# Kernel optimization log

Hardware: AMD Instinct MI355X
Metric: run time of the kernel (lower is better)

## Reference

```python
import jax, jax.numpy as jnp
import numpy as np

B, T, S, A = 4, 10, 6, 6
HID, L, IMG = 512, 6, 128
NCH = 16  # spatial-softmax channels
_px, _py = np.meshgrid(np.linspace(-1.0, 1.0, IMG), np.linspace(-1.0, 1.0, IMG))
POSX = jnp.asarray(_px.reshape(-1), jnp.float32)
POSY = jnp.asarray(_py.reshape(-1), jnp.float32)


def _conv_relu(x, w, b):
    y = jax.lax.conv_general_dilated(x, w, (1, 1), 'SAME',
                                     dimension_numbers=('NCHW', 'OIHW', 'NCHW'))
    return jax.nn.relu(y + b[None, :, None, None])


def _cnn_ss(x, ws, bs):
    for w, b in zip(ws, bs):
        x = _conv_relu(x, w, b)
    n = x.shape[0]
    attn = jax.nn.softmax(x.reshape(n, NCH, -1), axis=-1)  # (n, 16, H*W)
    ex = attn @ POSX  # (n, 16)
    ey = attn @ POSY
    return jnp.stack([ex, ey], axis=-1).reshape(n, 2 * NCH)  # (n, 32)


def _lstm_cell(x, h, c, wih, whh, bih, bhh):
    g = x @ wih.T + bih + h @ whh.T + bhh
    i, f, gg, o = jnp.split(g, 4, axis=-1)  # torch LSTMCell gate order i,f,g,o
    c2 = jax.nn.sigmoid(f) * c + jax.nn.sigmoid(i) * jnp.tanh(gg)
    h2 = jax.nn.sigmoid(o) * jnp.tanh(c2)
    return h2, c2


def setup_inputs() -> dict:
    key = jax.random.key(0)
    ks = iter(jax.random.split(key, 64))

    def nrm(shape, s=0.05):
        return jax.random.normal(next(ks), shape, dtype=jnp.float32) * s

    inp = {
        'seq_img_main': nrm((B, T, 3, IMG, IMG), 1.0),
        'seq_img_secondary': nrm((B, T, 3, IMG, IMG), 1.0),
        'seq_states': nrm((B, T, S), 1.0),
    }
    chans = [(32, 3), (64, 32), (128, 64), (16, 128)]
    for cam in ('m', 's'):
        for j, (o, ci) in enumerate(chans):
            inp[f'{cam}_w{j}'] = nrm((o, ci, 3, 3))
            inp[f'{cam}_b{j}'] = nrm((o,))
    in0, inr = S + 64, HID + 64  # 70 and 576
    inp['wih0'] = nrm((4 * HID, in0)); inp['whh0'] = nrm((4 * HID, HID))
    inp['bih0'] = nrm((4 * HID,)); inp['bhh0'] = nrm((4 * HID,))
    inp['wih_r'] = nrm((L - 1, 4 * HID, inr)); inp['whh_r'] = nrm((L - 1, 4 * HID, HID))
    inp['bih_r'] = nrm((L - 1, 4 * HID)); inp['bhh_r'] = nrm((L - 1, 4 * HID))
    inp['out_w'] = nrm((A, inr)); inp['out_b'] = nrm((A,))
    return inp


def reference(seq_img_main, seq_img_secondary, seq_states,
              m_w0, m_b0, m_w1, m_b1, m_w2, m_b2, m_w3, m_b3,
              s_w0, s_b0, s_w1, s_b1, s_w2, s_b2, s_w3, s_b3,
              wih0, whh0, bih0, bhh0, wih_r, whh_r, bih_r, bhh_r,
              out_w, out_b):
    b, t = seq_img_main.shape[:2]
    fm = _cnn_ss(seq_img_main.reshape(b * t, 3, IMG, IMG),
                 [m_w0, m_w1, m_w2, m_w3], [m_b0, m_b1, m_b2, m_b3])
    fs = _cnn_ss(seq_img_secondary.reshape(b * t, 3, IMG, IMG),
                 [s_w0, s_w1, s_w2, s_w3], [s_b0, s_b1, s_b2, s_b3])
    img = jnp.concatenate([fm, fs], axis=-1).reshape(b, t, 64)  # (B,T,64)

    h0 = jnp.zeros((L, b, HID), jnp.float32)
    c0 = jnp.zeros((L, b, HID), jnp.float32)

    def step(carry, xt):
        h, c = carry
        st, im = xt  # (B,S), (B,64)
        x = jnp.concatenate([st, im], axis=-1)
        hn, cn = _lstm_cell(x, h[0], c[0], wih0, whh0, bih0, bhh0)
        hs, cs = [hn], [cn]
        for l in range(L - 1):
            x = jnp.concatenate([hs[-1], im], axis=-1)
            hl, cl = _lstm_cell(x, h[l + 1], c[l + 1],
                                wih_r[l], whh_r[l], bih_r[l], bhh_r[l])
            hs.append(hl); cs.append(cl)
        out = jnp.concatenate([hs[-1], im], axis=-1) @ out_w.T + out_b
        return (jnp.stack(hs), jnp.stack(cs)), out

    _, outs = jax.lax.scan(step, (h0, c0),
                           (seq_states.transpose(1, 0, 2), img.transpose(1, 0, 2)))
    return outs.transpose(1, 0, 2)  # (B,T,A)
```

## Files before the change

kernel.cpp:

```cpp
#include <hip/hip_runtime.h>
#include <hip/hip_bf16.h>
#include <math.h>

typedef __hip_bfloat16 bf16;
typedef short bf16x8 __attribute__((ext_vector_type(8)));
typedef float f32x4 __attribute__((ext_vector_type(4)));

static constexpr int HWPX = 16384;

__device__ inline float sigmoidf_(float x) { return 1.0f / (1.0f + expf(-x)); }
__device__ inline float bflo(unsigned u) { return __uint_as_float(u << 16); }
__device__ inline float bfhi(unsigned u) { return __uint_as_float(u & 0xffff0000u); }
__device__ inline int swz(int x) { return (x ^ (x >> 2)) & 3; }

__device__ inline void gll16(const bf16* g, short* l) {
    __builtin_amdgcn_global_load_lds(
        (const __attribute__((address_space(1))) void*)g,
        (__attribute__((address_space(3))) void*)l, 16, 0, 0);
}

__global__ __launch_bounds__(256) void prep_lstm_k(
    const float* __restrict__ wih0, const float* __restrict__ whh0,
    const float* __restrict__ wihr, const float* __restrict__ whhr,
    bf16* __restrict__ d0, bf16* __restrict__ d1,
    bf16* __restrict__ d2, bf16* __restrict__ d3)
{
    const size_t nA = 2048ull * 72, nB = 2048ull * 512;
    const size_t nC = 5ull * 2048 * 576, nD = 5ull * 2048 * 512;
    for (size_t i = blockIdx.x * 256ull + threadIdx.x; i < nA + nB + nC + nD;
         i += (size_t)gridDim.x * 256) {
        if (i < nA) {
            int c = (int)(i % 72), r = (int)(i / 72);
            d0[i] = __float2bfloat16(c < 70 ? wih0[(size_t)r * 70 + c] : 0.f);
        } else if (i < nA + nB) {
            size_t k = i - nA; d1[k] = __float2bfloat16(whh0[k]);
        } else if (i < nA + nB + nC) {
            size_t k = i - nA - nB; d2[k] = __float2bfloat16(wihr[k]);
        } else {
            size_t k = i - nA - nB - nC; d3[k] = __float2bfloat16(whhr[k]);
        }
    }
}

struct ConvW {
    const float* src[8];
    bf16* dst[8];
};

__global__ __launch_bounds__(256) void prep_conv_k(ConvW a)
{
    const int sizes[4] = {3072, 18432, 73728, 18432};
    const int cins[4] = {3, 32, 64, 128};
    const int couts[4] = {32, 64, 128, 16};
    int total = 2 * 113664;
    for (int idx = blockIdx.x * 256 + threadIdx.x; idx < total; idx += gridDim.x * 256) {
        int i = idx, cam = 0;
        if (i >= 113664) { cam = 1; i -= 113664; }
        int layer = 0;
        while (layer < 3 && i >= sizes[layer]) { i -= sizes[layer]; ++layer; }
        const float* w = a.src[cam * 4 + layer];
        bf16* d = a.dst[cam * 4 + layer];
        if (layer == 0) {
            int k = i & 31, co = (i >> 5) & 31, ky = i >> 10;
            int kx = k >> 3, c = k & 7;
            float v = (kx < 3 && c < 3) ? w[((co * 3 + c) * 3 + ky) * 3 + kx] : 0.f;
            d[i] = __float2bfloat16(v);
        } else {
            int CIN = cins[layer], COUT = couts[layer], KC = CIN / 32;
            int e = i & 7;
            int t2 = i >> 3;
            int co = t2 % COUT;
            int t3 = t2 / COUT;
            int q = t3 & 3;
            int t4 = t3 >> 2;
            int kc = t4 % KC;
            int tap = t4 / KC;
            d[i] = __float2bfloat16(w[((size_t)(co * CIN + kc * 32 + q * 8 + e)) * 9 + tap]);
        }
    }
}

__global__ __launch_bounds__(256) void conv0_nhwc(
    const float* __restrict__ srcm, const float* __restrict__ srcs,
    const bf16* __restrict__ w0m, const bf16* __restrict__ w0s,
    const float* __restrict__ bm, const float* __restrict__ bs,
    bf16* __restrict__ out, int c0)
{
    const int y = blockIdx.x;
    const int cam = blockIdx.y;
    const int img = blockIdx.z;
    const int ci_ = cam * gridDim.z + img;
    const float* inImg = (cam ? srcs : srcm) + (size_t)(c0 + img) * 3 * HWPX;
    const bf16* wT0 = cam ? w0s : w0m;
    const float* bias = cam ? bs : bm;
    const int tid = threadIdx.x;
    const int wave = tid >> 6, lane = tid & 63;
    const int wm = wave & 1, wn = wave >> 1;
    const int q = lane >> 4, n16 = lane & 15;

    __shared__ short smem[3 * 130 * 16];

    for (int d = tid; d < 3 * 130; d += 256) {
        int x = d % 130, r = d / 130;
        int yy = y + r - 1, xx = x - 1;
        bf16 v8[8];
#pragma unroll
        for (int c = 0; c < 8; ++c) v8[c] = __float2bfloat16(0.f);
        if ((unsigned)yy < 128u && (unsigned)xx < 128u) {
            int o = yy * 128 + xx;
            v8[0] = __float2bfloat16(inImg[o]);
            v8[1] = __float2bfloat16(inImg[HWPX + o]);
            v8[2] = __float2bfloat16(inImg[2 * HWPX + o]);
        }
        *(bf16x8*)(void*)&smem[(r * 130 + x) * 16] = *(bf16x8*)(void*)v8;
        *(bf16x8*)(void*)&smem[(r * 130 + x) * 16 + 8] = (bf16x8)0;
    }
    __syncthreads();

    f32x4 acc[4];
#pragma unroll
    for (int nt = 0; nt < 4; ++nt) acc[nt] = f32x4{0.f, 0.f, 0.f, 0.f};

    const int co = wm * 16 + n16;
#pragma unroll
    for (int ky = 0; ky < 3; ++ky) {
        bf16x8 aF = *(const bf16x8*)(const void*)(wT0 + ((size_t)(ky * 32 + co) * 32) + q * 8);
#pragma unroll
        for (int nt = 0; nt < 4; ++nt) {
            int x = (wn * 4 + nt) * 16 + n16;
            int off = (q < 3) ? (ky * 130 + x + q) * 16 : (ky * 130 + x) * 16 + 8;
            bf16x8 bF = *(const bf16x8*)(const void*)&smem[off];
            acc[nt] = __builtin_amdgcn_mfma_f32_16x16x32_bf16(aF, bF, acc[nt], 0, 0, 0);
        }
    }

    int co0 = wm * 16 + q * 4;
#pragma unroll
    for (int nt = 0; nt < 4; ++nt) {
        int x = (wn * 4 + nt) * 16 + n16;
        bf16 tmp[4];
#pragma unroll
        for (int r = 0; r < 4; ++r) {
            float v = acc[nt][r] + bias[co0 + r];
            tmp[r] = __float2bfloat16(v > 0.f ? v : 0.f);
        }
        *reinterpret_cast<uint2*>(out + ((size_t)ci_ * HWPX + y * 128 + x) * 32 + co0)
            = *reinterpret_cast<uint2*>(tmp);
    }
}

template <int CIN, int COUT>
__global__ __launch_bounds__(256, 4) void conv2r(
    const bf16* __restrict__ in, const bf16* __restrict__ wTm,
    const bf16* __restrict__ wTs, const float* __restrict__ bm,
    const float* __restrict__ bs, bf16* __restrict__ out,
    const char* __restrict__ zpage)
{
    constexpr int KC = CIN / 32;
    constexpr int NB = (KC > 1) ? 2 : 1;
    constexpr int MW = COUT / 32;
    constexpr int SLOTS = 4 * 264;

    const int y0 = (blockIdx.x >> 1) * 2;
    const int x0 = (blockIdx.x & 1) * 64;
    const int cam = blockIdx.y;
    const int img = blockIdx.z;
    const int ci_ = cam * gridDim.z + img;
    const bf16* wT = cam ? wTs : wTm;
    const float* bias = cam ? bs : bm;
    const int tid = threadIdx.x;
    const int wave = tid >> 6, lane = tid & 63;
    const int wrow = wave >> 1, wm = wave & 1;
    const int q = lane >> 4, n16 = lane & 15;

    __shared__ short smem[NB][SLOTS * 8];
    const bf16* inImg = in + (size_t)ci_ * HWPX * CIN;

    const bf16* sptr[5];
#pragma unroll
    for (int it = 0; it < 5; ++it) {
        int s = it * 256 + tid;
        int r = s / 264, s2 = s - r * 264;
        int sx = s2 >> 2;
        int g = (s2 & 3) ^ swz(sx);
        int yy = y0 + r - 1, xx = x0 + sx - 1;
        bool ok = (s < SLOTS) && ((unsigned)yy < 128u) && ((unsigned)xx < 128u);
        sptr[it] = ok ? inImg + ((size_t)yy * 128 + xx) * CIN + g * 8
                      : (const bf16*)(zpage + (tid & 255) * 16);
    }
    auto stage = [&](int kc, int buf) {
#pragma unroll
        for (int it = 0; it < 5; ++it) {
            if (it * 256 + tid < SLOTS)
                gll16(sptr[it] + kc * 32, &smem[buf][it * 2048 + wave * 512]);
        }
    };

    f32x4 acc[MW][4];
#pragma unroll
    for (int mt = 0; mt < MW; ++mt)
#pragma unroll
        for (int nt = 0; nt < 4; ++nt) acc[mt][nt] = f32x4{0.f, 0.f, 0.f, 0.f};

    stage(0, 0);
    for (int kc = 0; kc < KC; ++kc) {
        __syncthreads();
        if (kc + 1 < KC) stage(kc + 1, (kc + 1) % NB);
        const short* sb = smem[kc % NB];
#pragma unroll
        for (int ky = 0; ky < 3; ++ky) {
#pragma unroll
            for (int kx = 0; kx < 3; ++kx) {
                bf16x8 aF[MW];
#pragma unroll
                for (int mt = 0; mt < MW; ++mt) {
                    int co = (wm * MW + mt) * 16 + n16;
                    aF[mt] = *(const bf16x8*)(const void*)(wT +
                        ((((size_t)(ky * 3 + kx) * KC + kc) * 4 + q) * COUT + co) * 8);
                }
#pragma unroll
                for (int nt = 0; nt < 4; ++nt) {
                    int xt = nt * 16 + n16 + kx;
                    int slot = (wrow + ky) * 264 + xt * 4 + (q ^ swz(xt));
                    bf16x8 bF = *(const bf16x8*)(const void*)&sb[slot * 8];
#pragma unroll
                    for (int mt = 0; mt < MW; ++mt)
                        acc[mt][nt] = __builtin_amdgcn_mfma_f32_16x16x32_bf16(
                            aF[mt], bF, acc[mt][nt], 0, 0, 0);
                }
            }
        }
    }

    const int y = y0 + wrow;
#pragma unroll
    for (int mt = 0; mt < MW; ++mt) {
        int co0 = (wm * MW + mt) * 16 + q * 4;
#pragma unroll
        for (int nt = 0; nt < 4; ++nt) {
            int x = x0 + nt * 16 + n16;
            bf16 tmp[4];
#pragma unroll
            for (int r = 0; r < 4; ++r) {
                float v = acc[mt][nt][r] + bias[co0 + r];
                tmp[r] = __float2bfloat16(v > 0.f ? v : 0.f);
            }
            *reinterpret_cast<uint2*>(out + ((size_t)ci_ * HWPX + y * 128 + x) * COUT + co0)
                = *reinterpret_cast<uint2*>(tmp);
        }
    }
}

__global__ __launch_bounds__(256, 6) void conv4_xs(
    const bf16* __restrict__ in, const bf16* __restrict__ wTm,
    const bf16* __restrict__ wTs, const float* __restrict__ bm,
    const float* __restrict__ bs,
    float* __restrict__ partial,
    const char* __restrict__ zpage, int c0)
{
    constexpr int CIN = 128, COUT = 16, KC = 4;
    constexpr int SLOTS = 3 * 66 * 4;
    const int y = blockIdx.x >> 1;
    const int xh = blockIdx.x & 1;
    const int x0 = xh * 64;
    const int cam = blockIdx.y;
    const int img = blockIdx.z;
    const int ci_ = cam * gridDim.z + img;
    const int gimg = cam * 40 + c0 + img;
    const bf16* wT = cam ? wTs : wTm;
    const float* bias = cam ? bs : bm;
    const int tid = threadIdx.x;
    const int wave = tid >> 6, lane = tid & 63;
    const int q = lane >> 4, n16 = lane & 15;

    __shared__ short smem[2][SLOTS * 8];
    __shared__ float sred[3][4][16];
    const bf16* inImg = in + (size_t)ci_ * HWPX * CIN;

    const bf16* sptr[4];
#pragma unroll
    for (int it = 0; it < 4; ++it) {
        int s = it * 256 + tid;
        int r = s / 264, s2 = s - r * 264;
        int sx = s2 >> 2;
        int g = (s2 & 3) ^ swz(sx);
        int yy = y + r - 1, xx = x0 + sx - 1;
        bool ok = (s < SLOTS) && ((unsigned)yy < 128u) && ((unsigned)xx < 128u);
        sptr[it] = ok ? inImg + ((size_t)yy * 128 + xx) * CIN + g * 8
                      : (const bf16*)(zpage + (tid & 255) * 16);
    }
    auto stage = [&](int kc, int buf) {
#pragma unroll
        for (int it = 0; it < 4; ++it) {
            if (it * 256 + tid < SLOTS)
                gll16(sptr[it] + kc * 32, &smem[buf][it * 2048 + wave * 512]);
        }
    };

    f32x4 acc = f32x4{0.f, 0.f, 0.f, 0.f};

    stage(0, 0);
    for (int kc = 0; kc < KC; ++kc) {
        __syncthreads();
        if (kc + 1 < KC) stage(kc + 1, (kc + 1) & 1);
        const short* sb = smem[kc & 1];
#pragma unroll
        for (int ky = 0; ky < 3; ++ky) {
#pragma unroll
            for (int kx = 0; kx < 3; ++kx) {
                bf16x8 aF = *(const bf16x8*)(const void*)(wT +
                    ((((size_t)(ky * 3 + kx) * KC + kc) * 4 + q) * COUT + n16) * 8);
                int xt = wave * 16 + n16 + kx;
                int slot = xt * 4 + (q ^ swz(xt));
                bf16x8 bF = *(const bf16x8*)(const void*)&sb[ky * 2112 + slot * 8];
                acc = __builtin_amdgcn_mfma_f32_16x16x32_bf16(aF, bF, acc, 0, 0, 0);
            }
        }
    }

    float v[4];
    int x = x0 + wave * 16 + n16;
    float px = -1.f + (2.f / 127.f) * x;
#pragma unroll
    for (int r = 0; r < 4; ++r) {
        float t = acc[r] + bias[q * 4 + r];
        v[r] = t > 0.f ? t : 0.f;
    }
    float M[4];
#pragma unroll
    for (int r = 0; r < 4; ++r) {
        M[r] = v[r];
        M[r] = fmaxf(M[r], __shfl_xor(M[r], 1));
        M[r] = fmaxf(M[r], __shfl_xor(M[r], 2));
        M[r] = fmaxf(M[r], __shfl_xor(M[r], 4));
        M[r] = fmaxf(M[r], __shfl_xor(M[r], 8));
    }
    if (n16 == 0)
#pragma unroll
        for (int r = 0; r < 4; ++r) sred[0][wave][q * 4 + r] = M[r];
    __syncthreads();
#pragma unroll
    for (int r = 0; r < 4; ++r) {
        M[r] = fmaxf(fmaxf(sred[0][0][q * 4 + r], sred[0][1][q * 4 + r]),
                     fmaxf(sred[0][2][q * 4 + r], sred[0][3][q * 4 + r]));
    }
    float s[4], sx[4];
#pragma unroll
    for (int r = 0; r < 4; ++r) {
        float e = expf(v[r] - M[r]);
        s[r] = e; sx[r] = e * px;
        s[r] += __shfl_xor(s[r], 1);  sx[r] += __shfl_xor(sx[r], 1);
        s[r] += __shfl_xor(s[r], 2);  sx[r] += __shfl_xor(sx[r], 2);
        s[r] += __shfl_xor(s[r], 4);  sx[r] += __shfl_xor(sx[r], 4);
        s[r] += __shfl_xor(s[r], 8);  sx[r] += __shfl_xor(sx[r], 8);
    }
    __syncthreads();
    if (n16 == 0)
#pragma unroll
        for (int r = 0; r < 4; ++r) {
            sred[1][wave][q * 4 + r] = s[r];
            sred[2][wave][q * 4 + r] = sx[r];
        }
    __syncthreads();
    if (tid < 16) {
        float S = sred[1][0][tid] + sred[1][1][tid] + sred[1][2][tid] + sred[1][3][tid];
        float SX = sred[2][0][tid] + sred[2][1][tid] + sred[2][2][tid] + sred[2][3][tid];
        float Mv = fmaxf(fmaxf(sred[0][0][tid], sred[0][1][tid]),
                         fmaxf(sred[0][2][tid], sred[0][3][tid]));
        float* pp = partial + (((size_t)gimg * 16 + tid) * 256 + (y * 2 + xh)) * 4;
        pp[0] = Mv; pp[1] = S; pp[2] = SX;
    }
}

__global__ __launch_bounds__(256) void ssmerge_k(
    const float* __restrict__ partial, float* __restrict__ featm,
    float* __restrict__ feats)
{
    const int img = blockIdx.x;
    const int cam = img / 40, li = img % 40;
    float* feat = cam ? feats : featm;
    const int tid = threadIdx.x;
    const int co = tid >> 4, s = tid & 15;
    const float* base = partial + ((size_t)img * 16 + co) * 256 * 4;
    float M = -1e30f, S = 0.f, SX = 0.f, SY = 0.f;
    for (int i = s; i < 256; i += 16) {
        float m = base[i * 4], sv = base[i * 4 + 1], sxv = base[i * 4 + 2];
        float py = -1.f + (2.f / 127.f) * (i >> 1);
        float Mn = fmaxf(M, m);
        float w0 = expf(M - Mn), w1 = expf(m - Mn);
        S = S * w0 + sv * w1;
        SX = SX * w0 + sxv * w1;
        SY = SY * w0 + sv * py * w1;
        M = Mn;
    }
#pragma unroll
    for (int mask = 1; mask < 16; mask <<= 1) {
        float Mo = __shfl_xor(M, mask), So = __shfl_xor(S, mask);
        float SXo = __shfl_xor(SX, mask), SYo = __shfl_xor(SY, mask);
        float Mn = fmaxf(M, Mo);
        float w0 = expf(M - Mn), w1 = expf(Mo - Mn);
        S = S * w0 + So * w1; SX = SX * w0 + SXo * w1; SY = SY * w0 + SYo * w1;
        M = Mn;
    }
    if (s == 0) {
        feat[(size_t)li * 32 + 2 * co] = SX / S;
        feat[(size_t)li * 32 + 2 * co + 1] = SY / S;
    }
}

__device__ inline float imgfeat(const float* featm, const float* feats,
                                int b, int t, int k)
{
    int idx = (b * 10 + t) * 32;
    return k < 32 ? featm[idx + k] : feats[idx + k - 32];
}

__global__ __launch_bounds__(256) void lstm_diag_k(
    const bf16* __restrict__ wih0p, const bf16* __restrict__ whh0b,
    const bf16* __restrict__ wihrb, const bf16* __restrict__ whhrb,
    const float* __restrict__ bih0, const float* __restrict__ bhh0,
    const float* __restrict__ bihr, const float* __restrict__ bhhr,
    const float* __restrict__ states,
    const float* __restrict__ featm, const float* __restrict__ feats,
    float* __restrict__ hAll, float* __restrict__ cAll,
    const float* __restrict__ out_w, const float* __restrict__ out_b,
    float* __restrict__ out, int d)
{
    const int l = blockIdx.y;
    const int tid = threadIdx.x;

    if (l == 6) {
        int t = d - 6;
        if (t < 0 || t >= 10 || blockIdx.x != 0) return;
        const float* h5 = hAll + ((size_t)(t + 1) * 6 + 5) * 2048;
        int p = tid >> 3, sub = tid & 7;
        if (p >= 24) return;
        int b = p / 6, a = p % 6;
        const float* wr = out_w + a * 576;
        float acc = 0.f;
        for (int k = sub; k < 512; k += 8) acc += wr[k] * h5[b * 512 + k];
        for (int k = sub; k < 64; k += 8) acc += wr[512 + k] * imgfeat(featm, feats, b, t, k);
        acc += __shfl_xor(acc, 1);
        acc += __shfl_xor(acc, 2);
        acc += __shfl_xor(acc, 4);
        if (sub == 0) out[(b * 10 + t) * 6 + a] = acc + out_b[a];
        return;
    }

    const int t = d - l;
    if (t < 0 || t >= 10) return;

    const bf16 *wih, *whh;
    const float *bih, *bhh;
    int K1;
    if (l == 0) { wih = wih0p; whh = whh0b; bih = bih0; bhh = bhh0; K1 = 72; }
    else {
        wih = wihrb + (size_t)(l - 1) * 2048 * 576;
        whh = whhrb + (size_t)(l - 1) * 2048 * 512;
        bih = bihr + (l - 1) * 2048;
        bhh = bhhr + (l - 1) * 2048;
        K1 = 576;
    }
    const float* hprev = (l == 0) ? nullptr : hAll + ((size_t)(t + 1) * 6 + (l - 1)) * 2048;
    const float* hold  = hAll + ((size_t)t * 6 + l) * 2048;
    float* hnew        = hAll + ((size_t)(t + 1) * 6 + l) * 2048;
    float* cst         = cAll + (size_t)l * 2048;

    const int XS = K1 + 512;
    __shared__ float xs[4 * 1088];
    for (int i = tid; i < 4 * XS; i += 256) {
        int b = i / XS, k = i - b * XS;
        float v;
        if (k < K1) {
            if (hprev) v = (k < 512) ? hprev[b * 512 + k]
                                     : imgfeat(featm, feats, b, t, k - 512);
            else       v = (k < 6) ? states[(b * 10 + t) * 6 + k]
                                   : (k < 70 ? imgfeat(featm, feats, b, t, k - 6) : 0.f);
        } else {
            v = hold[b * 512 + (k - K1)];
        }
        xs[b * XS + k] = v;
    }
    __syncthreads();

    const int b = tid >> 6;
    const int jloc = (tid >> 4) & 3;
    const int sub = tid & 15;
    const int j = blockIdx.x * 4 + jloc;
    const float* xb = xs + b * XS;
    const float* hp = xb + K1;
    float dg[4] = {0.f, 0.f, 0.f, 0.f};
    const int nb1 = K1 >> 3;
#pragma unroll
    for (int r = 0; r < 4; ++r) {
        const uint4* w1 = reinterpret_cast<const uint4*>(wih + (size_t)(j + r * 512) * K1);
        for (int g = sub; g < nb1; g += 16) {
            uint4 u = w1[g]; const float* xp = xb + g * 8;
            dg[r] += bflo(u.x) * xp[0] + bfhi(u.x) * xp[1] + bflo(u.y) * xp[2] + bfhi(u.y) * xp[3]
                   + bflo(u.z) * xp[4] + bfhi(u.z) * xp[5] + bflo(u.w) * xp[6] + bfhi(u.w) * xp[7];
        }
        const uint4* w2 = reinterpret_cast<const uint4*>(whh + (size_t)(j + r * 512) * 512);
        for (int g = sub; g < 64; g += 16) {
            uint4 u = w2[g]; const float* xp = hp + g * 8;
            dg[r] += bflo(u.x) * xp[0] + bfhi(u.x) * xp[1] + bflo(u.y) * xp[2] + bfhi(u.y) * xp[3]
                   + bflo(u.z) * xp[4] + bfhi(u.z) * xp[5] + bflo(u.w) * xp[6] + bfhi(u.w) * xp[7];
        }
    }
#pragma unroll
    for (int r = 0; r < 4; ++r) {
        dg[r] += __shfl_xor(dg[r], 1);
        dg[r] += __shfl_xor(dg[r], 2);
        dg[r] += __shfl_xor(dg[r], 4);
        dg[r] += __shfl_xor(dg[r], 8);
    }
    if (sub == 0) {
        float gi = dg[0] + bih[j] + bhh[j];
        float gf = dg[1] + bih[j + 512] + bhh[j + 512];
        float gg = dg[2] + bih[j + 1024] + bhh[j + 1024];
        float go = dg[3] + bih[j + 1536] + bhh[j + 1536];
        float cp = cst[b * 512 + j];
        float c2 = sigmoidf_(gf) * cp + sigmoidf_(gi) * tanhf(gg);
        float h2 = sigmoidf_(go) * tanhf(c2);
        cst[b * 512 + j] = c2;
        hnew[b * 512 + j] = h2;
    }
}

extern "C" void kernel_launch(void* const* d_in, const int* in_sizes, int n_in,
                              void* d_out, int out_size, void* d_ws, size_t ws_size,
                              hipStream_t stream)
{
    const float* seq_m = (const float*)d_in[0];
    const float* seq_s = (const float*)d_in[1];
    const float* states = (const float*)d_in[2];
    const float *cw[2][4], *cb[2][4];
    for (int cam = 0; cam < 2; ++cam)
        for (int j = 0; j < 4; ++j) {
            cw[cam][j] = (const float*)d_in[3 + cam * 8 + j * 2];
            cb[cam][j] = (const float*)d_in[3 + cam * 8 + j * 2 + 1];
        }
    const float* wih0  = (const float*)d_in[19];
    const float* whh0  = (const float*)d_in[20];
    const float* bih0  = (const float*)d_in[21];
    const float* bhh0  = (const float*)d_in[22];
    const float* wih_r = (const float*)d_in[23];
    const float* whh_r = (const float*)d_in[24];
    const float* bih_r = (const float*)d_in[25];
    const float* bhh_r = (const float*)d_in[26];
    const float* out_w = (const float*)d_in[27];
    const float* out_b = (const float*)d_in[28];
    float* out = (float*)d_out;

    char* wsc = (char*)d_ws;
    auto carve = [&](size_t bytes) {
        char* p = wsc;
        wsc += (bytes + 255) & ~(size_t)255;
        return p;
    };
    float* featm = (float*)carve(40 * 32 * 4);
    float* feats = (float*)carve(40 * 32 * 4);
    float* hAll  = (float*)carve((size_t)11 * 6 * 2048 * 4);
    float* cAll  = (float*)carve((size_t)6 * 2048 * 4);
    char*  zpage = carve(8192);
    float* partial = (float*)carve((size_t)80 * 16 * 256 * 4 * 4);
    const int wtElts[4] = {3072, 18432, 73728, 18432};
    bf16* wT[2][4];
    for (int cam = 0; cam < 2; ++cam)
        for (int j = 0; j < 4; ++j) wT[cam][j] = (bf16*)carve(wtElts[j] * 2);
    bf16* wih0p = (bf16*)carve((size_t)2048 * 72 * 2);
    bf16* whh0b = (bf16*)carve((size_t)2048 * 512 * 2);
    bf16* wihrb = (bf16*)carve((size_t)5 * 2048 * 576 * 2);
    bf16* whhrb = (bf16*)carve((size_t)5 * 2048 * 512 * 2);

    size_t used = (size_t)(wsc - (char*)d_ws);
    size_t rem = ws_size > used ? ws_size - used : 0;
    int CHI = 1;
    const int cands[7] = {20, 10, 8, 5, 4, 2, 1};
    for (int i = 0; i < 7; ++i) {
        size_t need = (size_t)2 * cands[i] * (128 + 64) * HWPX * 2;
        if (need <= rem) { CHI = cands[i]; break; }
    }
    bf16* bufA = (bf16*)carve((size_t)2 * CHI * HWPX * 128 * 2);
    bf16* bufB = (bf16*)carve((size_t)2 * CHI * HWPX * 64 * 2);

    hipMemsetAsync(hAll, 0, 6 * 2048 * 4, stream);
    hipMemsetAsync(cAll, 0, 6 * 2048 * 4, stream);
    hipMemsetAsync(zpage, 0, 8192, stream);

    prep_lstm_k<<<2048, 256, 0, stream>>>(wih0, whh0, wih_r, whh_r,
                                          wih0p, whh0b, wihrb, whhrb);
    ConvW cwArg;
    for (int cam = 0; cam < 2; ++cam)
        for (int j = 0; j < 4; ++j) {
            cwArg.src[cam * 4 + j] = cw[cam][j];
            cwArg.dst[cam * 4 + j] = wT[cam][j];
        }
    prep_conv_k<<<888, 256, 0, stream>>>(cwArg);

    for (int c0 = 0; c0 < 40; c0 += CHI) {
        int ch = (40 - c0) < CHI ? (40 - c0) : CHI;
        conv0_nhwc<<<dim3(128, 2, ch), 256, 0, stream>>>(
            seq_m, seq_s, wT[0][0], wT[1][0], cb[0][0], cb[1][0], bufA, c0);
        conv2r<32, 64><<<dim3(128, 2, ch), 256, 0, stream>>>(
            bufA, wT[0][1], wT[1][1], cb[0][1], cb[1][1], bufB, zpage);
        conv2r<64, 128><<<dim3(128, 2, ch), 256, 0, stream>>>(
            bufB, wT[0][2], wT[1][2], cb[0][2], cb[1][2], bufA, zpage);
        conv4_xs<<<dim3(256, 2, ch), 256, 0, stream>>>(
            bufA, wT[0][3], wT[1][3], cb[0][3], cb[1][3], partial, zpage, c0);
    }
    ssmerge_k<<<80, 256, 0, stream>>>(partial, featm, feats);

    for (int d = 0; d < 16; ++d) {
        lstm_diag_k<<<dim3(128, 7), 256, 0, stream>>>(
            wih0p, whh0b, wihrb, whhrb, bih0, bhh0, bih_r, bhh_r,
            states, featm, feats, hAll, cAll, out_w, out_b, out, d);
    }
}
```

Measured before the change: 1.139 ms.

## Fuse LSTM diagonal launches into one cooperative kernel with grid sync

```diff
diff --git a/kernel.cpp b/kernel.cpp
--- a/kernel.cpp
+++ b/kernel.cpp
@@ -1,6 +1,9 @@
 #include <hip/hip_runtime.h>
 #include <hip/hip_bf16.h>
+#include <hip/hip_cooperative_groups.h>
 #include <math.h>
+
+namespace cg = cooperative_groups;
 
 typedef __hip_bfloat16 bf16;
 typedef short bf16x8 __attribute__((ext_vector_type(8)));
@@ -526,6 +529,130 @@
     }
 }
 
+__global__ __launch_bounds__(256) void lstm_coop_k(
+    const bf16* __restrict__ wih0p, const bf16* __restrict__ whh0b,
+    const bf16* __restrict__ wihrb, const bf16* __restrict__ whhrb,
+    const float* __restrict__ bih0, const float* __restrict__ bhh0,
+    const float* __restrict__ bihr, const float* __restrict__ bhhr,
+    const float* __restrict__ states,
+    const float* __restrict__ featm, const float* __restrict__ feats,
+    float* __restrict__ hAll, float* __restrict__ cAll,
+    const float* __restrict__ out_w, const float* __restrict__ out_b,
+    float* __restrict__ out)
+{
+    cg::grid_group grid = cg::this_grid();
+    const int l = blockIdx.x >> 7;
+    const int bx = blockIdx.x & 127;
+    const int tid = threadIdx.x;
+
+    const bf16 *wih = nullptr, *whh = nullptr;
+    const float *bih = nullptr, *bhh = nullptr;
+    int K1 = 0;
+    if (l == 0) { wih = wih0p; whh = whh0b; bih = bih0; bhh = bhh0; K1 = 72; }
+    else if (l < 6) {
+        wih = wihrb + (size_t)(l - 1) * 2048 * 576;
+        whh = whhrb + (size_t)(l - 1) * 2048 * 512;
+        bih = bihr + (l - 1) * 2048;
+        bhh = bhhr + (l - 1) * 2048;
+        K1 = 576;
+    }
+    const int XS = K1 + 512;
+    float* cst = cAll + (size_t)l * 2048;
+
+    __shared__ float xs[4 * 1088];
+
+    for (int d = 0; d < 16; ++d) {
+        if (l == 6) {
+            int t = d - 6;
+            if (t >= 0 && t < 10 && bx == 0) {
+                const float* h5 = hAll + ((size_t)(t + 1) * 6 + 5) * 2048;
+                int p = tid >> 3, sub = tid & 7;
+                if (p < 24) {
+                    int b = p / 6, a = p % 6;
+                    const float* wr = out_w + a * 576;
+                    float acc = 0.f;
+                    for (int k = sub; k < 512; k += 8) acc += wr[k] * h5[b * 512 + k];
+                    for (int k = sub; k < 64; k += 8)
+                        acc += wr[512 + k] * imgfeat(featm, feats, b, t, k);
+                    acc += __shfl_xor(acc, 1);
+                    acc += __shfl_xor(acc, 2);
+                    acc += __shfl_xor(acc, 4);
+                    if (sub == 0) out[(b * 10 + t) * 6 + a] = acc + out_b[a];
+                }
+            }
+        } else {
+            const int t = d - l;
+            if (t >= 0 && t < 10) {
+                const float* hprev = (l == 0) ? nullptr
+                                   : hAll + ((size_t)(t + 1) * 6 + (l - 1)) * 2048;
+                const float* hold  = hAll + ((size_t)t * 6 + l) * 2048;
+                float* hnew        = hAll + ((size_t)(t + 1) * 6 + l) * 2048;
+
+                for (int i = tid; i < 4 * XS; i += 256) {
+                    int b = i / XS, k = i - b * XS;
+                    float v;
+                    if (k < K1) {
+                        if (hprev) v = (k < 512) ? hprev[b * 512 + k]
+                                                 : imgfeat(featm, feats, b, t, k - 512);
+                        else       v = (k < 6) ? states[(b * 10 + t) * 6 + k]
+                                               : (k < 70 ? imgfeat(featm, feats, b, t, k - 6) : 0.f);
+                    } else {
+                        v = hold[b * 512 + (k - K1)];
+                    }
+                    xs[b * XS + k] = v;
+                }
+                __syncthreads();
+
+                const int b = tid >> 6;
+                const int jloc = (tid >> 4) & 3;
+                const int sub = tid & 15;
+                const int j = bx * 4 + jloc;
+                const float* xb = xs + b * XS;
+                const float* hp = xb + K1;
+                float dg[4] = {0.f, 0.f, 0.f, 0.f};
+                const int nb1 = K1 >> 3;
+#pragma unroll
+                for (int r = 0; r < 4; ++r) {
+                    const uint4* w1 = reinterpret_cast<const uint4*>(wih + (size_t)(j + r * 512) * K1);
+                    for (int g = sub; g < nb1; g += 16) {
+                        uint4 u = w1[g]; const float* xp = xb + g * 8;
+                        dg[r] += bflo(u.x) * xp[0] + bfhi(u.x) * xp[1] + bflo(u.y) * xp[2] + bfhi(u.y) * xp[3]
+                               + bflo(u.z) * xp[4] + bfhi(u.z) * xp[5] + bflo(u.w) * xp[6] + bfhi(u.w) * xp[7];
+                    }
+                    const uint4* w2 = reinterpret_cast<const uint4*>(whh + (size_t)(j + r * 512) * 512);
+                    for (int g = sub; g < 64; g += 16) {
+                        uint4 u = w2[g]; const float* xp = hp + g * 8;
+                        dg[r] += bflo(u.x) * xp[0] + bfhi(u.x) * xp[1] + bflo(u.y) * xp[2] + bfhi(u.y) * xp[3]
+                               + bflo(u.z) * xp[4] + bfhi(u.z) * xp[5] + bflo(u.w) * xp[6] + bfhi(u.w) * xp[7];
+                    }
+                }
+#pragma unroll
+                for (int r = 0; r < 4; ++r) {
+                    dg[r] += __shfl_xor(dg[r], 1);
+                    dg[r] += __shfl_xor(dg[r], 2);
+                    dg[r] += __shfl_xor(dg[r], 4);
+                    dg[r] += __shfl_xor(dg[r], 8);
+                }
+                if (sub == 0) {
+                    float gi = dg[0] + bih[j] + bhh[j];
+                    float gf = dg[1] + bih[j + 512] + bhh[j + 512];
+                    float gg = dg[2] + bih[j + 1024] + bhh[j + 1024];
+                    float go = dg[3] + bih[j + 1536] + bhh[j + 1536];
+                    float cp = cst[b * 512 + j];
+                    float c2 = sigmoidf_(gf) * cp + sigmoidf_(gi) * tanhf(gg);
+                    float h2 = sigmoidf_(go) * tanhf(c2);
+                    cst[b * 512 + j] = c2;
+                    hnew[b * 512 + j] = h2;
+                }
+            }
+        }
+        if (d < 15) {
+            __threadfence();
+            grid.sync();
+        }
+    }
+}
+
 extern "C" void kernel_launch(void* const* d_in, const int* in_sizes, int n_in,
                               void* d_out, int out_size, void* d_ws, size_t ws_size,
                               hipStream_t stream)
@@ -575,8 +702,8 @@
     size_t used = (size_t)(wsc - (char*)d_ws);
     size_t rem = ws_size > used ? ws_size - used : 0;
     int CHI = 1;
-    const int cands[7] = {20, 10, 8, 5, 4, 2, 1};
-    for (int i = 0; i < 7; ++i) {
+    const int cands[6] = {10, 8, 5, 4, 2, 1};
+    for (int i = 0; i < 6; ++i) {
         size_t need = (size_t)2 * cands[i] * (128 + 64) * HWPX * 2;
         if (need <= rem) { CHI = cands[i]; break; }
     }
@@ -610,9 +737,21 @@
     }
     ssmerge_k<<<80, 256, 0, stream>>>(partial, featm, feats);
 
-    for (int d = 0; d < 16; ++d) {
-        lstm_diag_k<<<dim3(128, 7), 256, 0, stream>>>(
-            wih0p, whh0b, wihrb, whhrb, bih0, bhh0, bih_r, bhh_r,
-            states, featm, feats, hAll, cAll, out_w, out_b, out, d);
-    }
-}
+    void* kargs[] = {
+        (void*)&wih0p, (void*)&whh0b, (void*)&wihrb, (void*)&whhrb,
+        (void*)&bih0, (void*)&bhh0, (void*)&bih_r, (void*)&bhh_r,
+        (void*)&states, (void*)&featm, (void*)&feats,
+        (void*)&hAll, (void*)&cAll,
+        (void*)&out_w, (void*)&out_b, (void*)&out
+    };
+    hipError_t ce = hipLaunchCooperativeKernel(
+        reinterpret_cast<void*>(lstm_coop_k), dim3(896), dim3(256),
+        kargs, 0, stream);
+    if (ce != hipSuccess) {
+        for (int d = 0; d < 16; ++d) {
+            lstm_diag_k<<<dim3(128, 7), 256, 0, stream>>>(
+                wih0p, whh0b, wihrb, whhrb, bih0, bhh0, bih_r, bhh_r,
+                states, featm, feats, hAll, cAll, out_w, out_b, out, d);
+        }
+    }
+}
```

Result: slower. 3.875 ms (+240.2%).

## Replace per-diagonal LSTM launches with persistent flag-synchronized pipeline kernel

Applied to the files above, without the earlier changes.

```diff
diff --git a/kernel.cpp b/kernel.cpp
--- a/kernel.cpp
+++ b/kernel.cpp
@@ -7,6 +7,7 @@
 typedef float f32x4 __attribute__((ext_vector_type(4)));
 
 static constexpr int HWPX = 16384;
+static constexpr int NBL  = 64;
 
 __device__ inline float sigmoidf_(float x) { return 1.0f / (1.0f + expf(-x)); }
 __device__ inline float bflo(unsigned u) { return __uint_as_float(u << 16); }
@@ -17,6 +18,19 @@
     __builtin_amdgcn_global_load_lds(
         (const __attribute__((address_space(1))) void*)g,
         (__attribute__((address_space(3))) void*)l, 16, 0, 0);
+}
+
+__device__ inline void flag_wait(int* p, int target) {
+    if (threadIdx.x == 0) {
+        while (__hip_atomic_load(p, __ATOMIC_ACQUIRE, __HIP_MEMORY_SCOPE_AGENT) < target)
+            __builtin_amdgcn_s_sleep(2);
+    }
+    __syncthreads();
+}
+__device__ inline void flag_post(int* p) {
+    __syncthreads();
+    if (threadIdx.x == 0)
+        __hip_atomic_fetch_add(p, 1, __ATOMIC_RELEASE, __HIP_MEMORY_SCOPE_AGENT);
 }
 
 __global__ __launch_bounds__(256) void prep_lstm_k(
@@ -415,7 +429,7 @@
     return k < 32 ? featm[idx + k] : feats[idx + k - 32];
 }
 
-__global__ __launch_bounds__(256) void lstm_diag_k(
+__global__ __launch_bounds__(256) void lstm_pipe_k(
     const bf16* __restrict__ wih0p, const bf16* __restrict__ whh0b,
     const bf16* __restrict__ wihrb, const bf16* __restrict__ whhrb,
     const float* __restrict__ bih0, const float* __restrict__ bhh0,
@@ -424,31 +438,34 @@
     const float* __restrict__ featm, const float* __restrict__ feats,
     float* __restrict__ hAll, float* __restrict__ cAll,
     const float* __restrict__ out_w, const float* __restrict__ out_b,
-    float* __restrict__ out, int d)
-{
-    const int l = blockIdx.y;
+    float* __restrict__ out, int* __restrict__ cnt)
+{
+    const int gb = blockIdx.x;
     const int tid = threadIdx.x;
 
-    if (l == 6) {
-        int t = d - 6;
-        if (t < 0 || t >= 10 || blockIdx.x != 0) return;
-        const float* h5 = hAll + ((size_t)(t + 1) * 6 + 5) * 2048;
-        int p = tid >> 3, sub = tid & 7;
-        if (p >= 24) return;
-        int b = p / 6, a = p % 6;
-        const float* wr = out_w + a * 576;
-        float acc = 0.f;
-        for (int k = sub; k < 512; k += 8) acc += wr[k] * h5[b * 512 + k];
-        for (int k = sub; k < 64; k += 8) acc += wr[512 + k] * imgfeat(featm, feats, b, t, k);
-        acc += __shfl_xor(acc, 1);
-        acc += __shfl_xor(acc, 2);
-        acc += __shfl_xor(acc, 4);
-        if (sub == 0) out[(b * 10 + t) * 6 + a] = acc + out_b[a];
+    if (gb == 6 * NBL) {
+        for (int t = 0; t < 10; ++t) {
+            flag_wait(&cnt[(5 * 10 + t) * 32], NBL);
+            const float* h5 = hAll + ((size_t)(t + 1) * 6 + 5) * 2048;
+            int p = tid >> 3, sub = tid & 7;
+            if (p < 24) {
+                int b = p / 6, a = p % 6;
+                const float* wr = out_w + a * 576;
+                float acc = 0.f;
+                for (int k = sub; k < 512; k += 8) acc += wr[k] * h5[b * 512 + k];
+                for (int k = sub; k < 64; k += 8)
+                    acc += wr[512 + k] * imgfeat(featm, feats, b, t, k);
+                acc += __shfl_xor(acc, 1);
+                acc += __shfl_xor(acc, 2);
+                acc += __shfl_xor(acc, 4);
+                if (sub == 0) out[(b * 10 + t) * 6 + a] = acc + out_b[a];
+            }
+        }
         return;
     }
 
-    const int t = d - l;
-    if (t < 0 || t >= 10) return;
+    const int l = gb / NBL;
+    const int bx = gb % NBL;
 
     const bf16 *wih, *whh;
     const float *bih, *bhh;
@@ -461,68 +478,78 @@
         bhh = bhhr + (l - 1) * 2048;
         K1 = 576;
     }
-    const float* hprev = (l == 0) ? nullptr : hAll + ((size_t)(t + 1) * 6 + (l - 1)) * 2048;
-    const float* hold  = hAll + ((size_t)t * 6 + l) * 2048;
-    float* hnew        = hAll + ((size_t)(t + 1) * 6 + l) * 2048;
-    float* cst         = cAll + (size_t)l * 2048;
-
     const int XS = K1 + 512;
+    float* cst = cAll + (size_t)l * 2048;
+
+    const int b = tid >> 6;
+    const int lane = tid & 63;
+    const int jloc = lane >> 3;
+    const int sub = lane & 7;
+    const int j = bx * 8 + jloc;
+    const int nb1 = K1 >> 3;
+
     __shared__ float xs[4 * 1088];
-    for (int i = tid; i < 4 * XS; i += 256) {
-        int b = i / XS, k = i - b * XS;
-        float v;
-        if (k < K1) {
-            if (hprev) v = (k < 512) ? hprev[b * 512 + k]
-                                     : imgfeat(featm, feats, b, t, k - 512);
-            else       v = (k < 6) ? states[(b * 10 + t) * 6 + k]
-                                   : (k < 70 ? imgfeat(featm, feats, b, t, k - 6) : 0.f);
-        } else {
-            v = hold[b * 512 + (k - K1)];
-        }
-        xs[b * XS + k] = v;
-    }
-    __syncthreads();
-
-    const int b = tid >> 6;
-    const int jloc = (tid >> 4) & 3;
-    const int sub = tid & 15;
-    const int j = blockIdx.x * 4 + jloc;
-    const float* xb = xs + b * XS;
-    const float* hp = xb + K1;
-    float dg[4] = {0.f, 0.f, 0.f, 0.f};
-    const int nb1 = K1 >> 3;
-#pragma unroll
-    for (int r = 0; r < 4; ++r) {
-        const uint4* w1 = reinterpret_cast<const uint4*>(wih + (size_t)(j + r * 512) * K1);
-        for (int g = sub; g < nb1; g += 16) {
-            uint4 u = w1[g]; const float* xp = xb + g * 8;
-            dg[r] += bflo(u.x) * xp[0] + bfhi(u.x) * xp[1] + bflo(u.y) * xp[2] + bfhi(u.y) * xp[3]
-                   + bflo(u.z) * xp[4] + bfhi(u.z) * xp[5] + bflo(u.w) * xp[6] + bfhi(u.w) * xp[7];
-        }
-        const uint4* w2 = reinterpret_cast<const uint4*>(whh + (size_t)(j + r * 512) * 512);
-        for (int g = sub; g < 64; g += 16) {
-            uint4 u = w2[g]; const float* xp = hp + g * 8;
-            dg[r] += bflo(u.x) * xp[0] + bfhi(u.x) * xp[1] + bflo(u.y) * xp[2] + bfhi(u.y) * xp[3]
-                   + bflo(u.z) * xp[4] + bfhi(u.z) * xp[5] + bflo(u.w) * xp[6] + bfhi(u.w) * xp[7];
-        }
-    }
-#pragma unroll
-    for (int r = 0; r < 4; ++r) {
-        dg[r] += __shfl_xor(dg[r], 1);
-        dg[r] += __shfl_xor(dg[r], 2);
-        dg[r] += __shfl_xor(dg[r], 4);
-        dg[r] += __shfl_xor(dg[r], 8);
-    }
-    if (sub == 0) {
-        float gi = dg[0] + bih[j] + bhh[j];
-        float gf = dg[1] + bih[j + 512] + bhh[j + 512];
-        float gg = dg[2] + bih[j + 1024] + bhh[j + 1024];
-        float go = dg[3] + bih[j + 1536] + bhh[j + 1536];
-        float cp = cst[b * 512 + j];
-        float c2 = sigmoidf_(gf) * cp + sigmoidf_(gi) * tanhf(gg);
-        float h2 = sigmoidf_(go) * tanhf(c2);
-        cst[b * 512 + j] = c2;
-        hnew[b * 512 + j] = h2;
+
+    for (int t = 0; t < 10; ++t) {
+        if (t > 0) flag_wait(&cnt[(l * 10 + t - 1) * 32], NBL);
+        if (l > 0) flag_wait(&cnt[((l - 1) * 10 + t) * 32], NBL);
+
+        const float* hprev = (l == 0) ? nullptr
+                           : hAll + ((size_t)(t + 1) * 6 + (l - 1)) * 2048;
+        const float* hold  = hAll + ((size_t)t * 6 + l) * 2048;
+        float* hnew        = hAll + ((size_t)(t + 1) * 6 + l) * 2048;
+
+        for (int i = tid; i < 4 * XS; i += 256) {
+            int bb = i / XS, k = i - bb * XS;
+            float v;
+            if (k < K1) {
+                if (hprev) v = (k < 512) ? hprev[bb * 512 + k]
+                                         : imgfeat(featm, feats, bb, t, k - 512);
+                else       v = (k < 6) ? states[(bb * 10 + t) * 6 + k]
+                                       : (k < 70 ? imgfeat(featm, feats, bb, t, k - 6) : 0.f);
+            } else {
+                v = hold[bb * 512 + (k - K1)];
+            }
+            xs[bb * XS + k] = v;
+        }
+        __syncthreads();
+
+        const float* xb = xs + b * XS;
+        const float* hp = xb + K1;
+        float dg[4] = {0.f, 0.f, 0.f, 0.f};
+#pragma unroll
+        for (int r = 0; r < 4; ++r) {
+            const uint4* w1 = reinterpret_cast<const uint4*>(wih + (size_t)(j + r * 512) * K1);
+            for (int g = sub; g < nb1; g += 8) {
+                uint4 u = w1[g]; const float* xp = xb + g * 8;
+                dg[r] += bflo(u.x) * xp[0] + bfhi(u.x) * xp[1] + bflo(u.y) * xp[2] + bfhi(u.y) * xp[3]
+                       + bflo(u.z) * xp[4] + bfhi(u.z) * xp[5] + bflo(u.w) * xp[6] + bfhi(u.w) * xp[7];
+            }
+            const uint4* w2 = reinterpret_cast<const uint4*>(whh + (size_t)(j + r * 512) * 512);
+            for (int g = sub; g < 64; g += 8) {
+                uint4 u = w2[g]; const float* xp = hp + g * 8;
+                dg[r] += bflo(u.x) * xp[0] + bfhi(u.x) * xp[1] + bflo(u.y) * xp[2] + bfhi(u.y) * xp[3]
+                       + bflo(u.z) * xp[4] + bfhi(u.z) * xp[5] + bflo(u.w) * xp[6] + bfhi(u.w) * xp[7];
+            }
+        }
+#pragma unroll
+        for (int r = 0; r < 4; ++r) {
+            dg[r] += __shfl_xor(dg[r], 1);
+            dg[r] += __shfl_xor(dg[r], 2);
+            dg[r] += __shfl_xor(dg[r], 4);
+        }
+        if (sub == 0) {
+            float gi = dg[0] + bih[j] + bhh[j];
+            float gf = dg[1] + bih[j + 512] + bhh[j + 512];
+            float gg = dg[2] + bih[j + 1024] + bhh[j + 1024];
+            float go = dg[3] + bih[j + 1536] + bhh[j + 1536];
+            float cp = cst[b * 512 + j];
+            float c2 = sigmoidf_(gf) * cp + sigmoidf_(gi) * tanhf(gg);
+            float h2 = sigmoidf_(go) * tanhf(c2);
+            cst[b * 512 + j] = c2;
+            hnew[b * 512 + j] = h2;
+        }
+        flag_post(&cnt[(l * 10 + t) * 32]);
     }
 }
 
@@ -562,6 +589,7 @@
     float* hAll  = (float*)carve((size_t)11 * 6 * 2048 * 4);
     float* cAll  = (float*)carve((size_t)6 * 2048 * 4);
     char*  zpage = carve(8192);
+    int*   lcnt  = (int*)carve((size_t)6 * 10 * 32 * 4);
     float* partial = (float*)carve((size_t)80 * 16 * 256 * 4 * 4);
     const int wtElts[4] = {3072, 18432, 73728, 18432};
     bf16* wT[2][4];
@@ -586,6 +614,7 @@
     hipMemsetAsync(hAll, 0, 6 * 2048 * 4, stream);
     hipMemsetAsync(cAll, 0, 6 * 2048 * 4, stream);
     hipMemsetAsync(zpage, 0, 8192, stream);
+    hipMemsetAsync(lcnt, 0, 6 * 10 * 32 * 4, stream);
 
     prep_lstm_k<<<2048, 256, 0, stream>>>(wih0, whh0, wih_r, whh_r,
                                           wih0p, whh0b, wihrb, whhrb);
@@ -610,9 +639,7 @@
     }
     ssmerge_k<<<80, 256, 0, stream>>>(partial, featm, feats);
 
-    for (int d = 0; d < 16; ++d) {
-        lstm_diag_k<<<dim3(128, 7), 256, 0, stream>>>(
-            wih0p, whh0b, wihrb, whhrb, bih0, bhh0, bih_r, bhh_r,
-            states, featm, feats, hAll, cAll, out_w, out_b, out, d);
-    }
-}
+    lstm_pipe_k<<<dim3(6 * NBL + 1), 256, 0, stream>>>(
+        wih0p, whh0b, wihrb, whhrb, bih0, bhh0, bih_r, bhh_r,
+        states, featm, feats, hAll, cAll, out_w, out_b, out, lcnt);
+}
```

Result: slower. 1.902 ms (+67.0%).
